# Optimization experiments

Measured on AMD Instinct MI355X. Metric: run time of the kernel, lower is better.

## Reference

```python
import jax, jax.numpy as jnp
import numpy as np

N, C, D = 32, 512, 2048
Q = 64          # num_query_tokens
H = 16          # num_attention_heads
DH = D // H     # head dim


def _mlp(z, w1, b1, w2, b2):
    # projection: Linear(D_r -> D_h), GELU (exact erf, torch default), Linear(D_h -> D_h)
    h = jax.nn.gelu(z @ w1 + b1, approximate=False)
    return h @ w2 + b2


def setup_inputs() -> dict:
    key = jax.random.key(0)
    ks = jax.random.split(key, 16)
    s = 0.02
    inp = {
        "x": jax.random.normal(ks[0], (N, C, D), dtype=jnp.float32),
        # projection MLP (shared by both experts since projector_type has no 'proj')
        "proj_w1": jax.random.normal(ks[1], (D, D), dtype=jnp.float32) * s,
        "proj_b1": jnp.zeros((D,), dtype=jnp.float32),
        "proj_w2": jax.random.normal(ks[2], (D, D), dtype=jnp.float32) * s,
        "proj_b2": jnp.zeros((D,), dtype=jnp.float32),
        # TextResampler (cross-attention with learned queries)
        "query_tokens": jax.random.normal(ks[3], (Q, D), dtype=jnp.float32) * s,
        "wq": jax.random.normal(ks[4], (D, D), dtype=jnp.float32) * s,
        "bq": jnp.zeros((D,), dtype=jnp.float32),
        "wk": jax.random.normal(ks[5], (D, D), dtype=jnp.float32) * s,
        "bk": jnp.zeros((D,), dtype=jnp.float32),
        "wv": jax.random.normal(ks[6], (D, D), dtype=jnp.float32) * s,
        "bv": jnp.zeros((D,), dtype=jnp.float32),
        "wo": jax.random.normal(ks[7], (D, D), dtype=jnp.float32) * s,
        "bo": jnp.zeros((D,), dtype=jnp.float32),
        # gate weight (zeros-init in module; random here to exercise routing)
        "w_gate": jax.random.normal(ks[8], (D, 2), dtype=jnp.float32) * s,
    }
    return inp


def reference(x, proj_w1, proj_b1, proj_w2, proj_b2, query_tokens,
              wq, bq, wk, bk, wv, bv, wo, bo, w_gate):
    n, c, d = x.shape
    # --- sampler: AdaptiveAvgPool2d((Q, D)); D dim is identity, C -> Q block means ---
    x_sampler = x.reshape(n, Q, c // Q, d).mean(axis=2)  # [N, Q, D]

    # --- expert 0: projection MLP on pooled tokens ---
    e0 = _mlp(x_sampler, proj_w1, proj_b1, proj_w2, proj_b2)  # [N, Q, D]

    # --- expert 1: TextResampler cross-attention over x, then shared projection ---
    q = (query_tokens @ wq + bq).reshape(Q, H, DH)            # [Q, H, DH]
    k = (x @ wk + bk).reshape(n, c, H, DH)                    # [N, C, H, DH]
    v = (x @ wv + bv).reshape(n, c, H, DH)
    scores = jnp.einsum("qhd,nchd->nhqc", q, k) / jnp.sqrt(jnp.float32(DH))
    attn = jax.nn.softmax(scores, axis=-1)                    # [N, H, Q, C]
    ctx = jnp.einsum("nhqc,nchd->nqhd", attn, v).reshape(n, Q, d)
    resampled = ctx @ wo + bo                                 # [N, Q, D]
    e1 = _mlp(resampled, proj_w1, proj_b1, proj_w2, proj_b2)  # [N, Q, D]

    # --- noisy top-k gating (eval path: clean logits) ---
    flat = x_sampler.reshape(n * Q, d)
    logits = jax.nn.softmax(flat @ w_gate, axis=1)            # [T, 2]
    top_vals, top_idx = jax.lax.top_k(logits, 2)              # min(k+1, num_experts)=2
    top_k_gates = top_vals / (top_vals.sum(axis=1, keepdims=True) + 1e-6)
    gates = jnp.zeros_like(logits).at[
        jnp.arange(n * Q)[:, None], top_idx].set(top_k_gates)
    gates = gates.reshape(n, Q, 2)

    # --- combine: matmul(stack(experts,-1), gates.unsqueeze(-1)).squeeze(-1) ---
    stacked = jnp.stack([e0, e1], axis=-1)                    # [N, Q, D, E]
    out = jnp.einsum("nqde,nqe->nqd", stacked, gates)
    return out.reshape(-1, d)                                 # [N*Q, D]
```

## Files before the change

kernel.cpp:

```cpp
#include <hip/hip_runtime.h>
#include <hip/hip_bf16.h>

typedef float f32x4 __attribute__((ext_vector_type(4)));
typedef short s16x8 __attribute__((ext_vector_type(8)));
typedef __hip_bfloat16 bf16;

#define NB 32
#define CB 512
#define DB 2048
#define QB 64
#define HB 16
#define DHB 128

static __device__ __forceinline__ void gload16(const void* g, void* l) {
  __builtin_amdgcn_global_load_lds(
      (const __attribute__((address_space(1))) void*)g,
      (__attribute__((address_space(3))) void*)l, 16, 0, 0);
}

static __device__ __forceinline__ unsigned short f2bf(float f) {
  bf16 b = __float2bfloat16(f);
  return *reinterpret_cast<unsigned short*>(&b);
}

static __device__ __forceinline__ float gelu_f(float z) {
  return 0.5f * z * (1.0f + erff(z * 0.7071067811865475f));
}

#define BAR2 do { asm volatile("" ::: "memory"); __builtin_amdgcn_s_barrier(); asm volatile("" ::: "memory"); } while (0)
#define VM2  asm volatile("s_waitcnt vmcnt(2)" ::: "memory")

__global__ void k_convpool(const float* __restrict__ x, bf16* __restrict__ x_bf,
                           bf16* __restrict__ tokens) {
  const int d0 = blockIdx.x * 1024 + threadIdx.x * 4;
  const int q = blockIdx.y, n = blockIdx.z;
  const size_t base = ((size_t)(n * CB + q * 8)) * DB + d0;
  float s0 = 0.f, s1 = 0.f, s2 = 0.f, s3 = 0.f;
#pragma unroll
  for (int j = 0; j < 8; ++j) {
    float4 v = *(const float4*)(x + base + (size_t)j * DB);
    s0 += v.x; s1 += v.y; s2 += v.z; s3 += v.w;
    ushort4 o; o.x = f2bf(v.x); o.y = f2bf(v.y); o.z = f2bf(v.z); o.w = f2bf(v.w);
    *(ushort4*)((unsigned short*)x_bf + base + (size_t)j * DB) = o;
  }
  ushort4 p;
  p.x = f2bf(s0 * 0.125f); p.y = f2bf(s1 * 0.125f);
  p.z = f2bf(s2 * 0.125f); p.w = f2bf(s3 * 0.125f);
  *(ushort4*)((unsigned short*)tokens + (size_t)2 * (n * QB + q) * DB + d0) = p;
}

__global__ void k_convert2(const float* __restrict__ a, unsigned short* __restrict__ oa, int na4,
                           const float* __restrict__ b, unsigned short* __restrict__ ob, int nb4) {
  int stride = gridDim.x * blockDim.x;
  int tot = na4 + nb4;
  for (int i = blockIdx.x * blockDim.x + threadIdx.x; i < tot; i += stride) {
    const float* src; unsigned short* dst; int k;
    if (i < na4) { src = a; dst = oa; k = i; } else { src = b; dst = ob; k = i - na4; }
    float4 v = ((const float4*)src)[k];
    ushort4 o;
    o.x = f2bf(v.x); o.y = f2bf(v.y); o.z = f2bf(v.z); o.w = f2bf(v.w);
    ((ushort4*)dst)[k] = o;
  }
}

__global__ void k_gate(const bf16* __restrict__ tokens, const float* __restrict__ wg,
                       float* __restrict__ gates, float* __restrict__ gsum) {
  int t = blockIdx.x * 4 + (threadIdx.x >> 6);
  int lane = threadIdx.x & 63;
  const bf16* row = tokens + (size_t)2 * t * DB;
  float z0 = 0.f, z1 = 0.f;
  for (int d = lane; d < DB; d += 64) {
    float v = __bfloat162float(row[d]);
    z0 += v * wg[d * 2];
    z1 += v * wg[d * 2 + 1];
  }
#pragma unroll
  for (int m = 32; m; m >>= 1) { z0 += __shfl_xor(z0, m, 64); z1 += __shfl_xor(z1, m, 64); }
  if (lane == 0) {
    float mx = fmaxf(z0, z1);
    float e0 = __expf(z0 - mx), e1 = __expf(z1 - mx);
    float s = e0 + e1;
    float p0 = e0 / s, p1 = e1 / s;
    float inv = 1.0f / (p0 + p1 + 1e-6f);
    float g0 = p0 * inv, g1 = p1 * inv;
    gates[t * 2] = g0;
    gates[t * 2 + 1] = g1;
    gsum[t] = g0 + g1;
  }
}

struct TP5 { const float* s[5]; bf16* d[5]; };
__global__ void k_transpose5(TP5 p) {
  __shared__ float t[32][33];
  const float* W = p.s[blockIdx.z];
  bf16* WT = p.d[blockIdx.z];
  int bx = blockIdx.x * 32;
  int by = blockIdx.y * 32;
  int tx = threadIdx.x;
  int ty = threadIdx.y;
  float4 v = *(const float4*)(W + (size_t)(by + ty) * DB + bx + tx * 4);
  t[ty][tx * 4 + 0] = v.x; t[ty][tx * 4 + 1] = v.y;
  t[ty][tx * 4 + 2] = v.z; t[ty][tx * 4 + 3] = v.w;
  __syncthreads();
  ushort4 o;
  o.x = f2bf(t[tx * 4 + 0][ty]);
  o.y = f2bf(t[tx * 4 + 1][ty]);
  o.z = f2bf(t[tx * 4 + 2][ty]);
  o.w = f2bf(t[tx * 4 + 3][ty]);
  *(ushort4*)((unsigned short*)WT + (size_t)(bx + ty) * DB + by + tx * 4) = o;
}

__global__ void k_qreduce(const float* __restrict__ qp, const float* __restrict__ bq,
                          bf16* __restrict__ qproj) {
  int i = blockIdx.x * 256 + threadIdx.x;
  const int S = QB * DB;
  float s = qp[i] + qp[i + S] + qp[i + 2 * S] + qp[i + 3 * S] + bq[i & (DB - 1)];
  qproj[i] = __float2bfloat16(s);
}

template <int EPI>
__global__ __launch_bounds__(512, 2) void k_gemm256(
    const bf16* __restrict__ A, int lda, long long sAb,
    const bf16* __restrict__ BT, int ldb, long long sBb,
    const float* __restrict__ bias, void* __restrict__ Cout, int ldc, long long sCb,
    int K, int ntiles) {
  __shared__ __align__(16) bf16 lds[2][2][256 * 64];

  int bid = blockIdx.x;
  { int c = gridDim.x >> 3; bid = (bid & 7) * c + (bid >> 3); }
  const int m0 = (bid / ntiles) * 256;
  const int n0 = (bid % ntiles) * 256;
  const int z = blockIdx.z;
  A += (size_t)z * sAb;
  BT += (size_t)z * sBb;

  const int tid = threadIdx.x;
  const int l = tid & 63, w = tid >> 6;
  const int wr = w >> 2, wc = w & 3;
  const int fr = l & 15, fg = l >> 4;

  const int rloc = w * 8 + (l >> 3);
  const int cswz = ((l & 7) ^ (l >> 3)) * 8;
  const bf16* Asw = A + cswz;
  const bf16* Bsw = BT + cswz;

  int rbA[4], rbB[4], ckb[2];
#pragma unroll
  for (int mi = 0; mi < 4; ++mi) rbA[mi] = (wr * 64 + mi * 16 + fr) * 128;
#pragma unroll
  for (int ni = 0; ni < 4; ++ni) rbB[ni] = ((ni >> 1) * 128 + wc * 32 + (ni & 1) * 16 + fr) * 128;
#pragma unroll
  for (int kk = 0; kk < 2; ++kk) ckb[kk] = ((kk * 4 + fg) ^ (fr & 7)) * 16;

  f32x4 acc[8][4] = {};
  s16x8 af[4], bfr[4][2];

  auto stg = [&](const bf16* srcsw, int ld, int row0, int kcol, char* dst) {
    gload16(srcsw + (size_t)(row0 + rloc) * ld + kcol, dst + w * 1024);
    gload16(srcsw + (size_t)(row0 + 64 + rloc) * ld + kcol, dst + 8192 + w * 1024);
  };

  stg(Asw, lda, m0, 0, (char*)&lds[0][0][0]);
  stg(Bsw, ldb, n0, 0, (char*)&lds[0][1][0]);
  stg(Bsw, ldb, n0 + 128, 0, (char*)&lds[0][1][0] + 16384);
  stg(Asw, lda, m0 + 128, 0, (char*)&lds[0][0][0] + 16384);
  asm volatile("s_waitcnt vmcnt(0)" ::: "memory");
  BAR2;

  const int NT = K >> 6;
  for (int t = 0; t < NT; ++t) {
    const int buf = t & 1;
    const char* Ab = (const char*)&lds[buf][0][0];
    const char* Bb = (const char*)&lds[buf][1][0];
    char* As = (char*)&lds[buf ^ 1][0][0];
    char* Bs = (char*)&lds[buf ^ 1][1][0];
    const int kn = (t + 1 < NT ? (t + 1) : 0) << 6;

    stg(Asw, lda, m0, kn, As);
#pragma unroll
    for (int mi = 0; mi < 4; ++mi) af[mi] = *(const s16x8*)(Ab + rbA[mi] + ckb[0]);
#pragma unroll
    for (int ni = 0; ni < 4; ++ni) bfr[ni][0] = *(const s16x8*)(Bb + rbB[ni] + ckb[0]);
    __builtin_amdgcn_s_setprio(1);
#pragma unroll
    for (int mi = 0; mi < 4; ++mi)
#pragma unroll
      for (int ni = 0; ni < 4; ++ni)
        acc[mi][ni] = __builtin_amdgcn_mfma_f32_16x16x32_bf16(af[mi], bfr[ni][0], acc[mi][ni], 0, 0, 0);
    __builtin_amdgcn_s_setprio(0);
    VM2;
    BAR2;

    stg(Bsw, ldb, n0, kn, Bs);
#pragma unroll
    for (int mi = 0; mi < 4; ++mi) af[mi] = *(const s16x8*)(Ab + 16384 + rbA[mi] + ckb[0]);
    __builtin_amdgcn_s_setprio(1);
#pragma unroll
    for (int mi = 0; mi < 4; ++mi)
#pragma unroll
      for (int ni = 0; ni < 4; ++ni)
        acc[4 + mi][ni] = __builtin_amdgcn_mfma_f32_16x16x32_bf16(af[mi], bfr[ni][0], acc[4 + mi][ni], 0, 0, 0);
    __builtin_amdgcn_s_setprio(0);

    stg(Bsw, ldb, n0 + 128, kn, Bs + 16384);
#pragma unroll
    for (int mi = 0; mi < 4; ++mi) af[mi] = *(const s16x8*)(Ab + rbA[mi] + ckb[1]);
#pragma unroll
    for (int ni = 0; ni < 4; ++ni) bfr[ni][1] = *(const s16x8*)(Bb + rbB[ni] + ckb[1]);
    __builtin_amdgcn_s_setprio(1);
#pragma unroll
    for (int mi = 0; mi < 4; ++mi)
#pragma unroll
      for (int ni = 0; ni < 4; ++ni)
        acc[mi][ni] = __builtin_amdgcn_mfma_f32_16x16x32_bf16(af[mi], bfr[ni][1], acc[mi][ni], 0, 0, 0);
    __builtin_amdgcn_s_setprio(0);

    stg(Asw, lda, m0 + 128, kn, As + 16384);
#pragma unroll
    for (int mi = 0; mi < 4; ++mi) af[mi] = *(const s16x8*)(Ab + 16384 + rbA[mi] + ckb[1]);
    __builtin_amdgcn_s_setprio(1);
#pragma unroll
    for (int mi = 0; mi < 4; ++mi)
#pragma unroll
      for (int ni = 0; ni < 4; ++ni)
        acc[4 + mi][ni] = __builtin_amdgcn_mfma_f32_16x16x32_bf16(af[mi], bfr[ni][1], acc[4 + mi][ni], 0, 0, 0);
    __builtin_amdgcn_s_setprio(0);
    VM2;
    BAR2;
  }

#pragma unroll
  for (int mi = 0; mi < 8; ++mi) {
    int row = m0 + (mi >> 2) * 128 + wr * 64 + (mi & 3) * 16 + fg * 4;
#pragma unroll
    for (int ni = 0; ni < 4; ++ni) {
      int col = n0 + (ni >> 1) * 128 + wc * 32 + (ni & 1) * 16 + fr;
      float bv = bias ? bias[col] : 0.f;
#pragma unroll
      for (int j = 0; j < 4; ++j) {
        float v = acc[mi][ni][j] + bv;
        size_t o = (size_t)z * sCb + (size_t)(row + j) * ldc + col;
        if (EPI == 0) {
          ((bf16*)Cout)[o] = __float2bfloat16(v);
        } else if (EPI == 1) {
          ((bf16*)Cout)[o] = __float2bfloat16(gelu_f(v));
        } else {
          ((float*)Cout)[o] = v;
        }
      }
    }
  }
}

template <int EPI>
__global__ __launch_bounds__(512, 2) void k_gemmH(
    const bf16* __restrict__ A, int lda,
    const bf16* __restrict__ BT, int ldb,
    const float* __restrict__ bias, void* __restrict__ Cout, int ldc,
    int K, int ntiles, const float* __restrict__ gates) {
  __shared__ __align__(16) bf16 ldsA[2][128 * 64];
  __shared__ __align__(16) bf16 ldsB[2][256 * 64];

  int bid = blockIdx.x;
  { int c = gridDim.x >> 3; bid = (bid & 7) * c + (bid >> 3); }
  const int m0 = (bid / ntiles) * 128;
  const int n0 = (bid % ntiles) * 256;

  const int tid = threadIdx.x;
  const int l = tid & 63, w = tid >> 6;
  const int wr = w >> 2, wc = w & 3;
  const int fr = l & 15, fg = l >> 4;

  const int rloc = w * 8 + (l >> 3);
  const int cswz = ((l & 7) ^ (l >> 3)) * 8;
  const bf16* Asw = A + cswz;
  const bf16* Bsw = BT + cswz;

  int rbA[4], rbB[4], ckb[2];
#pragma unroll
  for (int mi = 0; mi < 4; ++mi) rbA[mi] = (wr * 64 + mi * 16 + fr) * 128;
#pragma unroll
  for (int ni = 0; ni < 4; ++ni) rbB[ni] = ((ni >> 1) * 128 + wc * 32 + (ni & 1) * 16 + fr) * 128;
#pragma unroll
  for (int kk = 0; kk < 2; ++kk) ckb[kk] = ((kk * 4 + fg) ^ (fr & 7)) * 16;

  f32x4 acc[4][4] = {};
  s16x8 af[4], blo[2][2], bhi[2][2];

  auto stg = [&](const bf16* srcsw, int ld, int row0, int kcol, char* dst) {
    gload16(srcsw + (size_t)(row0 + rloc) * ld + kcol, dst + w * 1024);
    gload16(srcsw + (size_t)(row0 + 64 + rloc) * ld + kcol, dst + 8192 + w * 1024);
  };

  stg(Asw, lda, m0, 0, (char*)&ldsA[0][0]);
  stg(Bsw, ldb, n0, 0, (char*)&ldsB[0][0]);
  stg(Bsw, ldb, n0 + 128, 0, (char*)&ldsB[0][0] + 16384);
  asm volatile("s_waitcnt vmcnt(0)" ::: "memory");
  BAR2;

  const int NT = K >> 6;
  for (int t = 0; t < NT; ++t) {
    const int buf = t & 1;
    const char* Ab = (const char*)&ldsA[buf][0];
    const char* Bb = (const char*)&ldsB[buf][0];
    char* As = (char*)&ldsA[buf ^ 1][0];
    char* Bs = (char*)&ldsB[buf ^ 1][0];
    const int kn = (t + 1 < NT ? (t + 1) : 0) << 6;

    stg(Asw, lda, m0, kn, As);
#pragma unroll
    for (int mi = 0; mi < 4; ++mi) af[mi] = *(const s16x8*)(Ab + rbA[mi] + ckb[0]);
#pragma unroll
    for (int ni = 0; ni < 2; ++ni) blo[ni][0] = *(const s16x8*)(Bb + rbB[ni] + ckb[0]);
    __builtin_amdgcn_s_setprio(1);
#pragma unroll
    for (int mi = 0; mi < 4; ++mi)
#pragma unroll
      for (int ni = 0; ni < 2; ++ni)
        acc[mi][ni] = __builtin_amdgcn_mfma_f32_16x16x32_bf16(af[mi], blo[ni][0], acc[mi][ni], 0, 0, 0);
    __builtin_amdgcn_s_setprio(0);
    VM2;
    BAR2;

    stg(Bsw, ldb, n0, kn, Bs);
#pragma unroll
    for (int ni = 0; ni < 2; ++ni) bhi[ni][0] = *(const s16x8*)(Bb + rbB[2 + ni] + ckb[0]);
    __builtin_amdgcn_s_setprio(1);
#pragma unroll
    for (int mi = 0; mi < 4; ++mi)
#pragma unroll
      for (int ni = 0; ni < 2; ++ni)
        acc[mi][2 + ni] = __builtin_amdgcn_mfma_f32_16x16x32_bf16(af[mi], bhi[ni][0], acc[mi][2 + ni], 0, 0, 0);
    __builtin_amdgcn_s_setprio(0);

    stg(Bsw, ldb, n0 + 128, kn, Bs + 16384);
#pragma unroll
    for (int mi = 0; mi < 4; ++mi) af[mi] = *(const s16x8*)(Ab + rbA[mi] + ckb[1]);
#pragma unroll
    for (int ni = 0; ni < 2; ++ni) blo[ni][1] = *(const s16x8*)(Bb + rbB[ni] + ckb[1]);
    __builtin_amdgcn_s_setprio(1);
#pragma unroll
    for (int mi = 0; mi < 4; ++mi)
#pragma unroll
      for (int ni = 0; ni < 2; ++ni)
        acc[mi][ni] = __builtin_amdgcn_mfma_f32_16x16x32_bf16(af[mi], blo[ni][1], acc[mi][ni], 0, 0, 0);
    __builtin_amdgcn_s_setprio(0);

#pragma unroll
    for (int ni = 0; ni < 2; ++ni) bhi[ni][1] = *(const s16x8*)(Bb + rbB[2 + ni] + ckb[1]);
    __builtin_amdgcn_s_setprio(1);
#pragma unroll
    for (int mi = 0; mi < 4; ++mi)
#pragma unroll
      for (int ni = 0; ni < 2; ++ni)
        acc[mi][2 + ni] = __builtin_amdgcn_mfma_f32_16x16x32_bf16(af[mi], bhi[ni][1], acc[mi][2 + ni], 0, 0, 0);
    __builtin_amdgcn_s_setprio(0);
    VM2;
    BAR2;
  }

#pragma unroll
  for (int mi = 0; mi < 4; ++mi) {
    int row = m0 + wr * 64 + mi * 16 + fg * 4;
#pragma unroll
    for (int ni = 0; ni < 4; ++ni) {
      int col = n0 + (ni >> 1) * 128 + wc * 32 + (ni & 1) * 16 + fr;
      float bv = bias ? bias[col] : 0.f;
      if (EPI == 3) {
#pragma unroll
        for (int j = 0; j < 4; j += 2) {
          int tk = (row + j) >> 1;
          float g0 = gates[tk * 2], g1 = gates[tk * 2 + 1];
          float v0 = gelu_f(acc[mi][ni][j] + bv);
          float v1 = gelu_f(acc[mi][ni][j + 1] + bv);
          ((bf16*)Cout)[(size_t)tk * ldc + col] = __float2bfloat16(g0 * v0 + g1 * v1);
        }
      } else {
#pragma unroll
        for (int j = 0; j < 4; ++j) {
          float v = acc[mi][ni][j] + bv;
          size_t o = (size_t)(row + j) * ldc + col;
          if (EPI == 0) ((bf16*)Cout)[o] = __float2bfloat16(v);
          else ((float*)Cout)[o] = v;
        }
      }
    }
  }
}

template <int EPI>
__global__ __launch_bounds__(256) void k_gemm(
    const bf16* __restrict__ A, int lda, long long sAb,
    const bf16* __restrict__ BT, int ldb, long long sBb,
    const float* __restrict__ bias, void* __restrict__ Cout, int ldc, long long sCb,
    int M, int K, const float* __restrict__ gsum) {
  __shared__ bf16 As[128 * 32];
  __shared__ bf16 Bs[128 * 32];
  const int z = blockIdx.z;
  A += (size_t)z * sAb;
  BT += (size_t)z * sBb;
  const int tid = threadIdx.x;
  const int lane = tid & 63, w = tid >> 6;
  const int m0 = blockIdx.x * 128, n0 = blockIdx.y * 128;
  const int wm = (w >> 1) * 64, wn = (w & 1) * 64;
  f32x4 acc[4][4] = {};

  const int srow = tid >> 2;
  const int scol = (tid & 3) * 8;
  int gr0 = m0 + srow;       if (gr0 > M - 1) gr0 = M - 1;
  int gr1 = m0 + 64 + srow;  if (gr1 > M - 1) gr1 = M - 1;
  const bf16* ag0 = A + (size_t)gr0 * lda + scol;
  const bf16* ag1 = A + (size_t)gr1 * lda + scol;
  const bf16* bg0 = BT + (size_t)(n0 + srow) * ldb + scol;
  const bf16* bg1 = BT + (size_t)(n0 + 64 + srow) * ldb + scol;
  char* lA = (char*)As + w * 1024;
  char* lB = (char*)Bs + w * 1024;

  const int fr = lane & 15, fk = (lane >> 4) * 8;

  for (int k0 = 0; k0 < K; k0 += 32) {
    __syncthreads();
    gload16(ag0 + k0, lA);
    gload16(ag1 + k0, lA + 4096);
    gload16(bg0 + k0, lB);
    gload16(bg1 + k0, lB + 4096);
    __syncthreads();
    s16x8 af[4], bfr[4];
#pragma unroll
    for (int i = 0; i < 4; ++i)
      af[i] = *(const s16x8*)(As + (wm + i * 16 + fr) * 32 + fk);
#pragma unroll
    for (int i = 0; i < 4; ++i)
      bfr[i] = *(const s16x8*)(Bs + (wn + i * 16 + fr) * 32 + fk);
#pragma unroll
    for (int mi = 0; mi < 4; ++mi)
#pragma unroll
      for (int ni = 0; ni < 4; ++ni)
        acc[mi][ni] = __builtin_amdgcn_mfma_f32_16x16x32_bf16(af[mi], bfr[ni], acc[mi][ni], 0, 0, 0);
  }

  const int fg4 = (lane >> 4) * 4;
#pragma unroll
  for (int mi = 0; mi < 4; ++mi) {
#pragma unroll
    for (int ni = 0; ni < 4; ++ni) {
      int col = n0 + wn + ni * 16 + fr;
      float bv = bias ? bias[col] : 0.f;
#pragma unroll
      for (int j = 0; j < 4; ++j) {
        int r = m0 + wm + mi * 16 + fg4 + j;
        if (r >= M) continue;
        size_t o = (size_t)z * sCb + (size_t)r * ldc + col;
        if (EPI == 0) {
          ((bf16*)Cout)[o] = __float2bfloat16(acc[mi][ni][j] + bv);
        } else if (EPI == 1) {
          ((bf16*)Cout)[o] = __float2bfloat16(gelu_f(acc[mi][ni][j] + bv));
        } else if (EPI == 2) {
          ((float*)Cout)[o] = acc[mi][ni][j] + bv;
        } else {
          ((float*)Cout)[o] = acc[mi][ni][j] + gsum[r] * bv;
        }
      }
    }
  }
}

__global__ __launch_bounds__(256) void k_attn(
    const bf16* __restrict__ S, const bf16* __restrict__ Vg, bf16* __restrict__ ctxg) {
  __shared__ bf16 vt[128 * 64];
  __shared__ bf16 pb[4][16 * 64];
  const int nh = blockIdx.x;
  const int n = nh >> 4, h = nh & 15;
  const int tid = threadIdx.x, lane = tid & 63, w = tid >> 6;
  const int fr = lane & 15, fg = lane >> 4;

  f32x4 ctx[8] = {};
  float mrow[4], lrow[4];
#pragma unroll
  for (int j = 0; j < 4; ++j) { mrow[j] = -1e30f; lrow[j] = 0.f; }

  const bf16* Srow = S + ((size_t)n * (HB * QB) + h * QB) * CB;
  const bf16* Vbase = Vg + (size_t)(n * CB) * DB + h * DHB;
  const float SC = 0.08838834764831845f;

  const int krow = tid >> 4;
  const int kcol = (tid & 15) * 8;

  for (int c0 = 0; c0 < CB; c0 += 64) {
    __syncthreads();
#pragma unroll
    for (int jj = 0; jj < 4; ++jj) {
      int cc = jj * 16 + krow;
      s16x8 vv = *(const s16x8*)(Vbase + (size_t)(c0 + cc) * DB + kcol);
#pragma unroll
      for (int i = 0; i < 8; ++i) {
        int d = kcol + i;
        int sc = cc ^ ((((d & 7) ^ ((d >> 3) & 7))) << 3);
        vt[(size_t)d * 64 + sc] = ((const bf16*)&vv)[i];
      }
    }

    f32x4 s4[4];
#pragma unroll
    for (int ci = 0; ci < 4; ++ci)
#pragma unroll
      for (int j = 0; j < 4; ++j)
        s4[ci][j] = __bfloat162float(Srow[(size_t)(w * 16 + fg * 4 + j) * CB + c0 + ci * 16 + fr]);

#pragma unroll
    for (int j = 0; j < 4; ++j) {
      float m = fmaxf(fmaxf(s4[0][j], s4[1][j]), fmaxf(s4[2][j], s4[3][j])) * SC;
#pragma unroll
      for (int msk = 1; msk < 16; msk <<= 1) m = fmaxf(m, __shfl_xor(m, msk, 16));
      float newm = fmaxf(mrow[j], m);
      float resc = __expf(mrow[j] - newm);
      mrow[j] = newm;
      float rsum = 0.f;
      int q = fg * 4 + j;
      int qx = ((q & 7) ^ (q >> 3)) << 3;
#pragma unroll
      for (int ci = 0; ci < 4; ++ci) {
        float p = __expf(s4[ci][j] * SC - newm);
        rsum += p;
        pb[w][q * 64 + ((ci * 16 + fr) ^ qx)] = __float2bfloat16(p);
      }
#pragma unroll
      for (int msk = 1; msk < 16; msk <<= 1) rsum += __shfl_xor(rsum, msk, 16);
      lrow[j] = lrow[j] * resc + rsum;
#pragma unroll
      for (int ni = 0; ni < 8; ++ni) ctx[ni][j] = ctx[ni][j] * resc;
    }
    __syncthreads();

#pragma unroll
    for (int kk2 = 0; kk2 < 2; ++kk2) {
      int pqx = ((fr & 7) ^ (fr >> 3)) << 3;
      s16x8 pa = *(const s16x8*)(&pb[w][fr * 64 + ((kk2 * 32 + fg * 8) ^ pqx)]);
#pragma unroll
      for (int ni = 0; ni < 8; ++ni) {
        int d = ni * 16 + fr;
        int dx = (((d & 7) ^ ((d >> 3) & 7))) << 3;
        s16x8 bv = *(const s16x8*)(vt + (size_t)d * 64 + ((kk2 * 32 + fg * 8) ^ dx));
        ctx[ni] = __builtin_amdgcn_mfma_f32_16x16x32_bf16(pa, bv, ctx[ni], 0, 0, 0);
      }
    }
  }

#pragma unroll
  for (int ni = 0; ni < 8; ++ni) {
#pragma unroll
    for (int j = 0; j < 4; ++j) {
      int q = w * 16 + fg * 4 + j;
      float v = ctx[ni][j] / lrow[j];
      ctxg[(size_t)(n * QB + q) * DB + h * DHB + ni * 16 + fr] = __float2bfloat16(v);
    }
  }
}

extern "C" void kernel_launch(void* const* d_in, const int* in_sizes, int n_in,
                              void* d_out, int out_size, void* d_ws, size_t ws_size,
                              hipStream_t stream) {
  const float* x  = (const float*)d_in[0];
  const float* w1 = (const float*)d_in[1];
  const float* b1 = (const float*)d_in[2];
  const float* w2 = (const float*)d_in[3];
  const float* b2 = (const float*)d_in[4];
  const float* qt = (const float*)d_in[5];
  const float* wq = (const float*)d_in[6];
  const float* bq = (const float*)d_in[7];
  const float* wk = (const float*)d_in[8];
  const float* wv = (const float*)d_in[10];
  const float* bv = (const float*)d_in[11];
  const float* wo = (const float*)d_in[12];
  const float* bo = (const float*)d_in[13];
  const float* wg = (const float*)d_in[14];
  float* out = (float*)d_out;

  char* ws = (char*)d_ws;
  size_t off = 0;
  auto alloc = [&](size_t bytes) {
    char* p = ws + off;
    off += (bytes + 255) & ~(size_t)255;
    return p;
  };
  const size_t XE = (size_t)NB * CB * DB;
  const size_t WE = (size_t)DB * DB;
  const size_t TE = (size_t)NB * QB * DB;

  bf16* x_bf   = (bf16*)alloc(XE * 2);
  bf16* V_bf   = (bf16*)alloc(XE * 2);
  bf16* wk_bf  = (bf16*)alloc(WE * 2);
  bf16* w1T    = (bf16*)alloc(WE * 2);
  bf16* w2T    = (bf16*)alloc(WE * 2);
  bf16* wvT    = (bf16*)alloc(WE * 2);
  bf16* wqT    = (bf16*)alloc(WE * 2);
  bf16* woT    = (bf16*)alloc(WE * 2);
  bf16* tokens = (bf16*)alloc(2 * TE * 2);
  bf16* hmix   = (bf16*)alloc(TE * 2);
  bf16* ctx_bf = (bf16*)alloc(TE * 2);
  bf16* qt_bf  = (bf16*)alloc((size_t)QB * DB * 2);
  bf16* qproj  = (bf16*)alloc((size_t)QB * DB * 2);
  float* qpart = (float*)alloc((size_t)4 * QB * DB * 4);
  bf16* qk     = (bf16*)alloc((size_t)HB * QB * DB * 2);
  bf16* Sbuf   = (bf16*)alloc((size_t)NB * HB * QB * CB * 2);
  float* gates = (float*)alloc((size_t)NB * QB * 2 * 4);
  float* gsum  = (float*)alloc((size_t)NB * QB * 4);
  (void)ws_size; (void)in_sizes; (void)n_in; (void)out_size;

  k_convpool<<<dim3(2, 64, 32), 256, 0, stream>>>(x, x_bf, tokens);
  k_convert2<<<1024, 256, 0, stream>>>(
      qt, (unsigned short*)qt_bf, (int)(QB * DB / 4),
      wk, (unsigned short*)wk_bf, (int)(WE / 4));
  k_gate<<<NB * QB / 4, 256, 0, stream>>>(tokens, wg, gates, gsum);

  TP5 tp;
  tp.s[0] = w1; tp.d[0] = w1T;
  tp.s[1] = w2; tp.d[1] = w2T;
  tp.s[2] = wv; tp.d[2] = wvT;
  tp.s[3] = wq; tp.d[3] = wqT;
  tp.s[4] = wo; tp.d[4] = woT;
  k_transpose5<<<dim3(64, 64, 5), dim3(8, 32), 0, stream>>>(tp);

  k_gemm<2><<<dim3(1, 16, 4), 256, 0, stream>>>(
      qt_bf, DB, 512, wqT, DB, 512, nullptr, qpart, DB, (long long)QB * DB, QB, 512, nullptr);
  k_qreduce<<<QB * DB / 256, 256, 0, stream>>>(qpart, bq, qproj);

  k_gemm<0><<<dim3(1, 16, HB), 256, 0, stream>>>(
      qproj, DB, DHB, wk_bf, DB, DHB, nullptr, qk, DB, (long long)QB * DB, QB, DHB, nullptr);

  k_gemm256<0><<<dim3(512, 1, 1), 512, 0, stream>>>(
      x_bf, DB, 0, wvT, DB, 0, bv, V_bf, DB, 0, DB, 8);

  k_gemm256<0><<<dim3(8, 1, NB), 512, 0, stream>>>(
      qk, DB, 0, x_bf, DB, (long long)CB * DB, nullptr,
      Sbuf, CB, (long long)HB * QB * CB, DB, 2);

  k_attn<<<NB * HB, 256, 0, stream>>>(Sbuf, V_bf, ctx_bf);

  k_gemm<0><<<dim3(16, 16, 1), 256, 0, stream>>>(
      ctx_bf, DB, 0, woT, DB, 0, bo, tokens + DB, 2 * DB, 0, 2048, DB, nullptr);

  k_gemmH<3><<<dim3(256, 1, 1), 512, 0, stream>>>(
      tokens, DB, w1T, DB, b1, hmix, DB, DB, 8, gates);

  k_gemm<4><<<dim3(16, 16, 1), 256, 0, stream>>>(
      hmix, DB, 0, w2T, DB, 0, b2, out, DB, 0, 2048, DB, gsum);
}
```

Measured before the change: 496.4 us.

## Fuse gating into pooling kernel and add 128x256 GEMM for V projection

The gate softmax is now computed inside the pooling kernel from the fp32 pooled sums, with one block per token, so the separate k_gate launch and its re-read of the tokens are gone. The V projection GEMM moves to a new k_gemmL kernel with 128x256 tiles, a K-step of 32 and less LDS, allowing more blocks per CU and doubling the grid to 1024 blocks. The smaller K-step waits on vmcnt(0) every iteration, which weakens load/compute overlap. The gate now uses unrounded fp32 pooled values instead of bf16 tokens, a slight numeric difference.

Result: slower. 525.4 us (+5.8%).

```diff
diff --git a/kernel.cpp b/kernel.cpp
--- a/kernel.cpp
+++ b/kernel.cpp
@@ -29,11 +29,14 @@
 
 #define BAR2 do { asm volatile("" ::: "memory"); __builtin_amdgcn_s_barrier(); asm volatile("" ::: "memory"); } while (0)
 #define VM2  asm volatile("s_waitcnt vmcnt(2)" ::: "memory")
-
-__global__ void k_convpool(const float* __restrict__ x, bf16* __restrict__ x_bf,
-                           bf16* __restrict__ tokens) {
-  const int d0 = blockIdx.x * 1024 + threadIdx.x * 4;
-  const int q = blockIdx.y, n = blockIdx.z;
+#define VM0  asm volatile("s_waitcnt vmcnt(0)" ::: "memory")
+
+__global__ __launch_bounds__(512) void k_convpool(
+    const float* __restrict__ x, bf16* __restrict__ x_bf, bf16* __restrict__ tokens,
+    const float* __restrict__ wg, float* __restrict__ gates, float* __restrict__ gsum) {
+  __shared__ float red[2][8];
+  const int q = blockIdx.x, n = blockIdx.y;
+  const int d0 = threadIdx.x * 4;
   const size_t base = ((size_t)(n * CB + q * 8)) * DB + d0;
   float s0 = 0.f, s1 = 0.f, s2 = 0.f, s3 = 0.f;
 #pragma unroll
@@ -43,10 +46,33 @@
     ushort4 o; o.x = f2bf(v.x); o.y = f2bf(v.y); o.z = f2bf(v.z); o.w = f2bf(v.w);
     *(ushort4*)((unsigned short*)x_bf + base + (size_t)j * DB) = o;
   }
+  s0 *= 0.125f; s1 *= 0.125f; s2 *= 0.125f; s3 *= 0.125f;
   ushort4 p;
-  p.x = f2bf(s0 * 0.125f); p.y = f2bf(s1 * 0.125f);
-  p.z = f2bf(s2 * 0.125f); p.w = f2bf(s3 * 0.125f);
+  p.x = f2bf(s0); p.y = f2bf(s1); p.z = f2bf(s2); p.w = f2bf(s3);
   *(ushort4*)((unsigned short*)tokens + (size_t)2 * (n * QB + q) * DB + d0) = p;
+
+  float4 wga = *(const float4*)(wg + d0 * 2);
+  float4 wgb = *(const float4*)(wg + d0 * 2 + 4);
+  float z0 = s0 * wga.x + s1 * wga.z + s2 * wgb.x + s3 * wgb.z;
+  float z1 = s0 * wga.y + s1 * wga.w + s2 * wgb.y + s3 * wgb.w;
+#pragma unroll
+  for (int m = 32; m; m >>= 1) { z0 += __shfl_xor(z0, m, 64); z1 += __shfl_xor(z1, m, 64); }
+  int wv = threadIdx.x >> 6;
+  if ((threadIdx.x & 63) == 0) { red[0][wv] = z0; red[1][wv] = z1; }
+  __syncthreads();
+  if (threadIdx.x == 0) {
+    float Z0 = 0.f, Z1 = 0.f;
+#pragma unroll
+    for (int i = 0; i < 8; ++i) { Z0 += red[0][i]; Z1 += red[1][i]; }
+    float mx = fmaxf(Z0, Z1);
+    float e0 = __expf(Z0 - mx), e1 = __expf(Z1 - mx);
+    float s = e0 + e1;
+    float p0 = e0 / s, p1 = e1 / s;
+    float inv = 1.0f / (p0 + p1 + 1e-6f);
+    int t = n * QB + q;
+    float g0 = p0 * inv, g1 = p1 * inv;
+    gates[t * 2] = g0; gates[t * 2 + 1] = g1; gsum[t] = g0 + g1;
+  }
 }
 
 __global__ void k_convert2(const float* __restrict__ a, unsigned short* __restrict__ oa, int na4,
@@ -60,32 +86,6 @@
     ushort4 o;
     o.x = f2bf(v.x); o.y = f2bf(v.y); o.z = f2bf(v.z); o.w = f2bf(v.w);
     ((ushort4*)dst)[k] = o;
-  }
-}
-
-__global__ void k_gate(const bf16* __restrict__ tokens, const float* __restrict__ wg,
-                       float* __restrict__ gates, float* __restrict__ gsum) {
-  int t = blockIdx.x * 4 + (threadIdx.x >> 6);
-  int lane = threadIdx.x & 63;
-  const bf16* row = tokens + (size_t)2 * t * DB;
-  float z0 = 0.f, z1 = 0.f;
-  for (int d = lane; d < DB; d += 64) {
-    float v = __bfloat162float(row[d]);
-    z0 += v * wg[d * 2];
-    z1 += v * wg[d * 2 + 1];
-  }
-#pragma unroll
-  for (int m = 32; m; m >>= 1) { z0 += __shfl_xor(z0, m, 64); z1 += __shfl_xor(z1, m, 64); }
-  if (lane == 0) {
-    float mx = fmaxf(z0, z1);
-    float e0 = __expf(z0 - mx), e1 = __expf(z1 - mx);
-    float s = e0 + e1;
-    float p0 = e0 / s, p1 = e1 / s;
-    float inv = 1.0f / (p0 + p1 + 1e-6f);
-    float g0 = p0 * inv, g1 = p1 * inv;
-    gates[t * 2] = g0;
-    gates[t * 2 + 1] = g1;
-    gsum[t] = g0 + g1;
   }
 }
 
@@ -119,16 +119,17 @@
 }
 
 template <int EPI>
-__global__ __launch_bounds__(512, 2) void k_gemm256(
+__global__ __launch_bounds__(512, 4) void k_gemmL(
     const bf16* __restrict__ A, int lda, long long sAb,
     const bf16* __restrict__ BT, int ldb, long long sBb,
     const float* __restrict__ bias, void* __restrict__ Cout, int ldc, long long sCb,
     int K, int ntiles) {
-  __shared__ __align__(16) bf16 lds[2][2][256 * 64];
+  __shared__ __align__(16) bf16 lA2[2][128 * 32];
+  __shared__ __align__(16) bf16 lB2[2][256 * 32];
 
   int bid = blockIdx.x;
   { int c = gridDim.x >> 3; bid = (bid & 7) * c + (bid >> 3); }
-  const int m0 = (bid / ntiles) * 256;
+  const int m0 = (bid / ntiles) * 128;
   const int n0 = (bid % ntiles) * 256;
   const int z = blockIdx.z;
   A += (size_t)z * sAb;
@@ -139,99 +140,68 @@
   const int wr = w >> 2, wc = w & 3;
   const int fr = l & 15, fg = l >> 4;
 
-  const int rloc = w * 8 + (l >> 3);
-  const int cswz = ((l & 7) ^ (l >> 3)) * 8;
-  const bf16* Asw = A + cswz;
-  const bf16* Bsw = BT + cswz;
-
-  int rbA[4], rbB[4], ckb[2];
-#pragma unroll
-  for (int mi = 0; mi < 4; ++mi) rbA[mi] = (wr * 64 + mi * 16 + fr) * 128;
-#pragma unroll
-  for (int ni = 0; ni < 4; ++ni) rbB[ni] = ((ni >> 1) * 128 + wc * 32 + (ni & 1) * 16 + fr) * 128;
-#pragma unroll
-  for (int kk = 0; kk < 2; ++kk) ckb[kk] = ((kk * 4 + fg) ^ (fr & 7)) * 16;
-
-  f32x4 acc[8][4] = {};
-  s16x8 af[4], bfr[4][2];
-
-  auto stg = [&](const bf16* srcsw, int ld, int row0, int kcol, char* dst) {
-    gload16(srcsw + (size_t)(row0 + rloc) * ld + kcol, dst + w * 1024);
-    gload16(srcsw + (size_t)(row0 + 64 + rloc) * ld + kcol, dst + 8192 + w * 1024);
+  const int sr = tid >> 2;
+  const int sa = (sr & 3) ^ ((sr >> 2) & 3);
+  const int scz = ((tid & 3) ^ sa) * 8;
+
+  int adA[4], adB[4];
+#pragma unroll
+  for (int mi = 0; mi < 4; ++mi) {
+    int r = wr * 64 + mi * 16 + fr;
+    adA[mi] = r * 64 + ((fg ^ ((r & 3) ^ ((r >> 2) & 3))) * 16);
+  }
+#pragma unroll
+  for (int ni = 0; ni < 4; ++ni) {
+    int r = (ni >> 1) * 128 + wc * 32 + (ni & 1) * 16 + fr;
+    adB[ni] = r * 64 + ((fg ^ ((r & 3) ^ ((r >> 2) & 3))) * 16);
+  }
+
+  f32x4 acc[4][4] = {};
+  s16x8 af[4], bf[4];
+
+  auto stgA = [&](int kcol, char* dst) {
+    gload16(A + (size_t)(m0 + sr) * lda + kcol + scz, dst + w * 1024);
   };
-
-  stg(Asw, lda, m0, 0, (char*)&lds[0][0][0]);
-  stg(Bsw, ldb, n0, 0, (char*)&lds[0][1][0]);
-  stg(Bsw, ldb, n0 + 128, 0, (char*)&lds[0][1][0] + 16384);
-  stg(Asw, lda, m0 + 128, 0, (char*)&lds[0][0][0] + 16384);
-  asm volatile("s_waitcnt vmcnt(0)" ::: "memory");
+  auto stgB = [&](int kcol, char* dst) {
+    gload16(BT + (size_t)(n0 + sr) * ldb + kcol + scz, dst + w * 1024);
+    gload16(BT + (size_t)(n0 + 128 + sr) * ldb + kcol + scz, dst + 8192 + w * 1024);
+  };
+
+  stgA(0, (char*)&lA2[0][0]);
+  stgB(0, (char*)&lB2[0][0]);
+  VM0;
   BAR2;
 
-  const int NT = K >> 6;
+  const int NT = K >> 5;
   for (int t = 0; t < NT; ++t) {
     const int buf = t & 1;
-    const char* Ab = (const char*)&lds[buf][0][0];
-    const char* Bb = (const char*)&lds[buf][1][0];
-    char* As = (char*)&lds[buf ^ 1][0][0];
-    char* Bs = (char*)&lds[buf ^ 1][1][0];
-    const int kn = (t + 1 < NT ? (t + 1) : 0) << 6;
-
-    stg(Asw, lda, m0, kn, As);
-#pragma unroll
-    for (int mi = 0; mi < 4; ++mi) af[mi] = *(const s16x8*)(Ab + rbA[mi] + ckb[0]);
-#pragma unroll
-    for (int ni = 0; ni < 4; ++ni) bfr[ni][0] = *(const s16x8*)(Bb + rbB[ni] + ckb[0]);
+    const char* Ab = (const char*)&lA2[buf][0];
+    const char* Bb = (const char*)&lB2[buf][0];
+    char* As = (char*)&lA2[buf ^ 1][0];
+    char* Bs = (char*)&lB2[buf ^ 1][0];
+    const int kn = (t + 1 < NT ? (t + 1) : 0) << 5;
+
+    stgA(kn, As);
+    stgB(kn, Bs);
+#pragma unroll
+    for (int mi = 0; mi < 4; ++mi) af[mi] = *(const s16x8*)(Ab + adA[mi]);
+#pragma unroll
+    for (int ni = 0; ni < 4; ++ni) bf[ni] = *(const s16x8*)(Bb + adB[ni]);
     __builtin_amdgcn_s_setprio(1);
 #pragma unroll
     for (int mi = 0; mi < 4; ++mi)
 #pragma unroll
       for (int ni = 0; ni < 4; ++ni)
-        acc[mi][ni] = __builtin_amdgcn_mfma_f32_16x16x32_bf16(af[mi], bfr[ni][0], acc[mi][ni], 0, 0, 0);
-    __builtin_amdgcn_s_setprio(0);
-    VM2;
+        acc[mi][ni] = __builtin_amdgcn_mfma_f32_16x16x32_bf16(af[mi], bf[ni], acc[mi][ni], 0, 0, 0);
+    __builtin_amdgcn_s_setprio(0);
+    VM0;
     BAR2;
-
-    stg(Bsw, ldb, n0, kn, Bs);
-#pragma unroll
-    for (int mi = 0; mi < 4; ++mi) af[mi] = *(const s16x8*)(Ab + 16384 + rbA[mi] + ckb[0]);
-    __builtin_amdgcn_s_setprio(1);
-#pragma unroll
-    for (int mi = 0; mi < 4; ++mi)
-#pragma unroll
-      for (int ni = 0; ni < 4; ++ni)
-        acc[4 + mi][ni] = __builtin_amdgcn_mfma_f32_16x16x32_bf16(af[mi], bfr[ni][0], acc[4 + mi][ni], 0, 0, 0);
-    __builtin_amdgcn_s_setprio(0);
-
-    stg(Bsw, ldb, n0 + 128, kn, Bs + 16384);
-#pragma unroll
-    for (int mi = 0; mi < 4; ++mi) af[mi] = *(const s16x8*)(Ab + rbA[mi] + ckb[1]);
-#pragma unroll
-    for (int ni = 0; ni < 4; ++ni) bfr[ni][1] = *(const s16x8*)(Bb + rbB[ni] + ckb[1]);
-    __builtin_amdgcn_s_setprio(1);
-#pragma unroll
-    for (int mi = 0; mi < 4; ++mi)
-#pragma unroll
-      for (int ni = 0; ni < 4; ++ni)
-        acc[mi][ni] = __builtin_amdgcn_mfma_f32_16x16x32_bf16(af[mi], bfr[ni][1], acc[mi][ni], 0, 0, 0);
-    __builtin_amdgcn_s_setprio(0);
-
-    stg(Asw, lda, m0 + 128, kn, As + 16384);
-#pragma unroll
-    for (int mi = 0; mi < 4; ++mi) af[mi] = *(const s16x8*)(Ab + 16384 + rbA[mi] + ckb[1]);
-    __builtin_amdgcn_s_setprio(1);
-#pragma unroll
-    for (int mi = 0; mi < 4; ++mi)
-#pragma unroll
-      for (int ni = 0; ni < 4; ++ni)
-        acc[4 + mi][ni] = __builtin_amdgcn_mfma_f32_16x16x32_bf16(af[mi], bfr[ni][1], acc[4 + mi][ni], 0, 0, 0);
-    __builtin_amdgcn_s_setprio(0);
-    VM2;
-    BAR2;
-  }
-
-#pragma unroll
-  for (int mi = 0; mi < 8; ++mi) {
-    int row = m0 + (mi >> 2) * 128 + wr * 64 + (mi & 3) * 16 + fg * 4;
+  }
+
+  const int fg4 = fg * 4;
+#pragma unroll
+  for (int mi = 0; mi < 4; ++mi) {
+    int row = m0 + wr * 64 + mi * 16 + fg4;
 #pragma unroll
     for (int ni = 0; ni < 4; ++ni) {
       int col = n0 + (ni >> 1) * 128 + wc * 32 + (ni & 1) * 16 + fr;
@@ -253,6 +223,140 @@
 }
 
 template <int EPI>
+__global__ __launch_bounds__(512, 2) void k_gemm256(
+    const bf16* __restrict__ A, int lda, long long sAb,
+    const bf16* __restrict__ BT, int ldb, long long sBb,
+    const float* __restrict__ bias, void* __restrict__ Cout, int ldc, long long sCb,
+    int K, int ntiles) {
+  __shared__ __align__(16) bf16 lds[2][2][256 * 64];
+
+  int bid = blockIdx.x;
+  { int c = gridDim.x >> 3; bid = (bid & 7) * c + (bid >> 3); }
+  const int m0 = (bid / ntiles) * 256;
+  const int n0 = (bid % ntiles) * 256;
+  const int z = blockIdx.z;
+  A += (size_t)z * sAb;
+  BT += (size_t)z * sBb;
+
+  const int tid = threadIdx.x;
+  const int l = tid & 63, w = tid >> 6;
+  const int wr = w >> 2, wc = w & 3;
+  const int fr = l & 15, fg = l >> 4;
+
+  const int rloc = w * 8 + (l >> 3);
+  const int cswz = ((l & 7) ^ (l >> 3)) * 8;
+  const bf16* Asw = A + cswz;
+  const bf16* Bsw = BT + cswz;
+
+  int rbA[4], rbB[4], ckb[2];
+#pragma unroll
+  for (int mi = 0; mi < 4; ++mi) rbA[mi] = (wr * 64 + mi * 16 + fr) * 128;
+#pragma unroll
+  for (int ni = 0; ni < 4; ++ni) rbB[ni] = ((ni >> 1) * 128 + wc * 32 + (ni & 1) * 16 + fr) * 128;
+#pragma unroll
+  for (int kk = 0; kk < 2; ++kk) ckb[kk] = ((kk * 4 + fg) ^ (fr & 7)) * 16;
+
+  f32x4 acc[8][4] = {};
+  s16x8 af[4], bfr[4][2];
+
+  auto stg = [&](const bf16* srcsw, int ld, int row0, int kcol, char* dst) {
+    gload16(srcsw + (size_t)(row0 + rloc) * ld + kcol, dst + w * 1024);
+    gload16(srcsw + (size_t)(row0 + 64 + rloc) * ld + kcol, dst + 8192 + w * 1024);
+  };
+
+  stg(Asw, lda, m0, 0, (char*)&lds[0][0][0]);
+  stg(Bsw, ldb, n0, 0, (char*)&lds[0][1][0]);
+  stg(Bsw, ldb, n0 + 128, 0, (char*)&lds[0][1][0] + 16384);
+  stg(Asw, lda, m0 + 128, 0, (char*)&lds[0][0][0] + 16384);
+  VM0;
+  BAR2;
+
+  const int NT = K >> 6;
+  for (int t = 0; t < NT; ++t) {
+    const int buf = t & 1;
+    const char* Ab = (const char*)&lds[buf][0][0];
+    const char* Bb = (const char*)&lds[buf][1][0];
+    char* As = (char*)&lds[buf ^ 1][0][0];
+    char* Bs = (char*)&lds[buf ^ 1][1][0];
+    const int kn = (t + 1 < NT ? (t + 1) : 0) << 6;
+
+    stg(Asw, lda, m0, kn, As);
+#pragma unroll
+    for (int mi = 0; mi < 4; ++mi) af[mi] = *(const s16x8*)(Ab + rbA[mi] + ckb[0]);
+#pragma unroll
+    for (int ni = 0; ni < 4; ++ni) bfr[ni][0] = *(const s16x8*)(Bb + rbB[ni] + ckb[0]);
+    __builtin_amdgcn_s_setprio(1);
+#pragma unroll
+    for (int mi = 0; mi < 4; ++mi)
+#pragma unroll
+      for (int ni = 0; ni < 4; ++ni)
+        acc[mi][ni] = __builtin_amdgcn_mfma_f32_16x16x32_bf16(af[mi], bfr[ni][0], acc[mi][ni], 0, 0, 0);
+    __builtin_amdgcn_s_setprio(0);
+    VM2;
+    BAR2;
+
+    stg(Bsw, ldb, n0, kn, Bs);
+#pragma unroll
+    for (int mi = 0; mi < 4; ++mi) af[mi] = *(const s16x8*)(Ab + 16384 + rbA[mi] + ckb[0]);
+    __builtin_amdgcn_s_setprio(1);
+#pragma unroll
+    for (int mi = 0; mi < 4; ++mi)
+#pragma unroll
+      for (int ni = 0; ni < 4; ++ni)
+        acc[4 + mi][ni] = __builtin_amdgcn_mfma_f32_16x16x32_bf16(af[mi], bfr[ni][0], acc[4 + mi][ni], 0, 0, 0);
+    __builtin_amdgcn_s_setprio(0);
+
+    stg(Bsw, ldb, n0 + 128, kn, Bs + 16384);
+#pragma unroll
+    for (int mi = 0; mi < 4; ++mi) af[mi] = *(const s16x8*)(Ab + rbA[mi] + ckb[1]);
+#pragma unroll
+    for (int ni = 0; ni < 4; ++ni) bfr[ni][1] = *(const s16x8*)(Bb + rbB[ni] + ckb[1]);
+    __builtin_amdgcn_s_setprio(1);
+#pragma unroll
+    for (int mi = 0; mi < 4; ++mi)
+#pragma unroll
+      for (int ni = 0; ni < 4; ++ni)
+        acc[mi][ni] = __builtin_amdgcn_mfma_f32_16x16x32_bf16(af[mi], bfr[ni][1], acc[mi][ni], 0, 0, 0);
+    __builtin_amdgcn_s_setprio(0);
+
+    stg(Asw, lda, m0 + 128, kn, As + 16384);
+#pragma unroll
+    for (int mi = 0; mi < 4; ++mi) af[mi] = *(const s16x8*)(Ab + 16384 + rbA[mi] + ckb[1]);
+    __builtin_amdgcn_s_setprio(1);
+#pragma unroll
+    for (int mi = 0; mi < 4; ++mi)
+#pragma unroll
+      for (int ni = 0; ni < 4; ++ni)
+        acc[4 + mi][ni] = __builtin_amdgcn_mfma_f32_16x16x32_bf16(af[mi], bfr[ni][1], acc[4 + mi][ni], 0, 0, 0);
+    __builtin_amdgcn_s_setprio(0);
+    VM2;
+    BAR2;
+  }
+
+#pragma unroll
+  for (int mi = 0; mi < 8; ++mi) {
+    int row = m0 + (mi >> 2) * 128 + wr * 64 + (mi & 3) * 16 + fg * 4;
+#pragma unroll
+    for (int ni = 0; ni < 4; ++ni) {
+      int col = n0 + (ni >> 1) * 128 + wc * 32 + (ni & 1) * 16 + fr;
+      float bv = bias ? bias[col] : 0.f;
+#pragma unroll
+      for (int j = 0; j < 4; ++j) {
+        float v = acc[mi][ni][j] + bv;
+        size_t o = (size_t)z * sCb + (size_t)(row + j) * ldc + col;
+        if (EPI == 0) {
+          ((bf16*)Cout)[o] = __float2bfloat16(v);
+        } else if (EPI == 1) {
+          ((bf16*)Cout)[o] = __float2bfloat16(gelu_f(v));
+        } else {
+          ((float*)Cout)[o] = v;
+        }
+      }
+    }
+  }
+}
+
+template <int EPI>
 __global__ __launch_bounds__(512, 2) void k_gemmH(
     const bf16* __restrict__ A, int lda,
     const bf16* __restrict__ BT, int ldb,
@@ -295,7 +399,7 @@
   stg(Asw, lda, m0, 0, (char*)&ldsA[0][0]);
   stg(Bsw, ldb, n0, 0, (char*)&ldsB[0][0]);
   stg(Bsw, ldb, n0 + 128, 0, (char*)&ldsB[0][0] + 16384);
-  asm volatile("s_waitcnt vmcnt(0)" ::: "memory");
+  VM0;
   BAR2;
 
   const int NT = K >> 6;
@@ -607,11 +711,10 @@
   float* gsum  = (float*)alloc((size_t)NB * QB * 4);
   (void)ws_size; (void)in_sizes; (void)n_in; (void)out_size;
 
-  k_convpool<<<dim3(2, 64, 32), 256, 0, stream>>>(x, x_bf, tokens);
+  k_convpool<<<dim3(64, 32), 512, 0, stream>>>(x, x_bf, tokens, wg, gates, gsum);
   k_convert2<<<1024, 256, 0, stream>>>(
       qt, (unsigned short*)qt_bf, (int)(QB * DB / 4),
       wk, (unsigned short*)wk_bf, (int)(WE / 4));
-  k_gate<<<NB * QB / 4, 256, 0, stream>>>(tokens, wg, gates, gsum);
 
   TP5 tp;
   tp.s[0] = w1; tp.d[0] = w1T;
@@ -628,7 +731,7 @@
   k_gemm<0><<<dim3(1, 16, HB), 256, 0, stream>>>(
       qproj, DB, DHB, wk_bf, DB, DHB, nullptr, qk, DB, (long long)QB * DB, QB, DHB, nullptr);
 
-  k_gemm256<0><<<dim3(512, 1, 1), 512, 0, stream>>>(
+  k_gemmL<0><<<dim3(1024, 1, 1), 512, 0, stream>>>(
       x_bf, DB, 0, wvT, DB, 0, bv, V_bf, DB, 0, DB, 8);
 
   k_gemm256<0><<<dim3(8, 1, NB), 512, 0, stream>>>(
```
